# Performance work log

Hardware: AMD Instinct MI355X
Metric: run time of the kernel (lower is better)

Reference implementation:

```python
import jax, jax.numpy as jnp
import numpy as np

OUT_FEATURES = 64
KERNEL_DIMS = 16


def setup_inputs() -> dict:
    key = jax.random.key(0)
    k1, k2, k3, k4 = jax.random.split(key, 4)
    N, L, F = 256, 64, 32            # in_features = L*F = 2048
    OK = OUT_FEATURES * KERNEL_DIMS  # 1024
    x = jax.random.normal(k1, (N, L, F), dtype=jnp.float32)
    W = jax.random.normal(k2, (OK, L * F), dtype=jnp.float32) * 0.02
    b = jax.random.normal(k3, (OK,), dtype=jnp.float32) * 0.02
    u = jax.random.normal(k4, (OK,), dtype=jnp.float32)
    return {"x": x, "W": W, "b": b, "u": u}


def _l2normalize(a, eps=1e-12):
    return a / (jnp.linalg.norm(a) + eps)


def reference(x, W, b, u):
    N, L, F = x.shape
    xf = x.reshape(N, L * F)
    # spectral norm: one power iteration (u, v detached, as in torch)
    W_ng = jax.lax.stop_gradient(W)
    v = _l2normalize(W_ng.T @ u)
    u_new = _l2normalize(W_ng @ v)
    sigma = u_new @ (W @ v)          # differentiable in W
    W_sn = W / sigma
    # projection: (N, out, k)
    m = (xf @ W_sn.T + b).reshape(N, OUT_FEATURES, KERNEL_DIMS)
    # all-pairs L1 distance over kernel dim -> (N, N, out)
    norm = jnp.abs(m[:, None, :, :] - m[None, :, :, :]).sum(-1)
    o_b = jnp.exp(-norm).sum(0) - 1.0          # (N, out); self term exp(0)=1 removed
    o_b = jnp.broadcast_to(o_b[:, None, :], (N, L, OUT_FEATURES))
    return jnp.concatenate([x, o_b], axis=-1)  # (N, L, F + out)
```

## Files before the change

kernel.cpp:

```cpp
#include <hip/hip_runtime.h>
#include <hip/hip_bf16.h>
#include <math.h>

#define KIN  2048
#define OKD  1024
#define NB   256
#define OUTF 64
#define KD   16

typedef float f32x4  __attribute__((ext_vector_type(4)));
typedef short bf16x4 __attribute__((ext_vector_type(4)));
typedef short bf16x8 __attribute__((ext_vector_type(8)));
typedef unsigned short u16x8 __attribute__((ext_vector_type(8)));

static __device__ __forceinline__ unsigned short f2bf(float f) {
    union { __hip_bfloat16 b; unsigned short u; } cv;
    cv.b = __float2bfloat16(f);
    return cv.u;
}
static __device__ __forceinline__ u16x8 pack8(float4 a, float4 b) {
    u16x8 r;
    r[0]=f2bf(a.x); r[1]=f2bf(a.y); r[2]=f2bf(a.z); r[3]=f2bf(a.w);
    r[4]=f2bf(b.x); r[5]=f2bf(b.y); r[6]=f2bf(b.z); r[7]=f2bf(b.w);
    return r;
}
static __device__ __forceinline__ float bf2f(unsigned short u) {
    union { unsigned int i; float f; } cv; cv.i = ((unsigned int)u) << 16; return cv.f;
}

__global__ __launch_bounds__(256) void k_stage1(const float* __restrict__ W,
        const float* __restrict__ u, const float* __restrict__ x,
        float* __restrict__ partial, unsigned short* __restrict__ Wb,
        unsigned short* __restrict__ xb, float4* __restrict__ out4) {
    int bid = blockIdx.x, tid = threadIdx.x;
    if (bid < 256) {
        int row0 = bid * 4;
        int c = tid * 8;
        float s[8];
#pragma unroll
        for (int i = 0; i < 8; ++i) s[i] = 0.f;
#pragma unroll
        for (int r = 0; r < 4; ++r) {
            int row = row0 + r;
            const float4* src = (const float4*)(W + (size_t)row * KIN + c);
            float4 f0 = src[0], f1 = src[1];
            *(u16x8*)(Wb + (size_t)row * KIN + c) = pack8(f0, f1);
            float uu = u[row];
            s[0] += f0.x * uu; s[1] += f0.y * uu; s[2] += f0.z * uu; s[3] += f0.w * uu;
            s[4] += f1.x * uu; s[5] += f1.y * uu; s[6] += f1.z * uu; s[7] += f1.w * uu;
        }
        float4* dst = (float4*)(partial + (size_t)bid * KIN + c);
        dst[0] = make_float4(s[0], s[1], s[2], s[3]);
        dst[1] = make_float4(s[4], s[5], s[6], s[7]);
    } else if (bid < 288) {
        int xc = bid - 256;
        const float4* x4 = (const float4*)x;
#pragma unroll
        for (int p = 0; p < 8; ++p) {
            int g = xc * 2048 + p * 256 + tid;
            float4 f0 = x4[(size_t)g * 2], f1 = x4[(size_t)g * 2 + 1];
            *((u16x8*)xb + g) = pack8(f0, f1);
        }
    } else {
        int xo = bid - 288;
        const float4* x4 = (const float4*)x;
#pragma unroll
        for (int p = 0; p < 4; ++p) {
            int i = xo * 1024 + p * 256 + tid;
            int r = i >> 3, c = i & 7;
            out4[(size_t)r * 24 + c] = x4[i];
        }
    }
}

__global__ __launch_bounds__(256) void k_vred(const float* __restrict__ partial,
                                              float* __restrict__ partial2) {
    int bid = blockIdx.x, tid = threadIdx.x;
    int bg = bid & 1, cg = bid >> 1;
    int col = cg * 256 + tid;
    float a = 0.f;
#pragma unroll 8
    for (int i = 0; i < 128; ++i)
        a += partial[(size_t)(bg * 128 + i) * KIN + col];
    partial2[bg * KIN + col] = a;
}

static __device__ __forceinline__ bf16x8 load_frag(const unsigned short* lds, int row, int k0) {
    int b0 = (row << 7) + (k0 << 1);
    b0 ^= (row & 7) << 4;
    bf16x4 lo = *(const bf16x4*)((const char*)lds + b0);
    bf16x4 hi = *(const bf16x4*)((const char*)lds + (b0 ^ 32));
    bf16x8 r;
    r[0]=lo[0]; r[1]=lo[1]; r[2]=lo[2]; r[3]=lo[3];
    r[4]=hi[0]; r[5]=hi[1]; r[6]=hi[2]; r[7]=hi[3];
    return r;
}

__global__ __launch_bounds__(256) void k_tg(const unsigned short* __restrict__ xb,
        const unsigned short* __restrict__ Wb, const float* __restrict__ partial2,
        float* __restrict__ tpart, float* __restrict__ P) {
    __shared__ unsigned short sAB[2][4096];
    __shared__ float part[4], part2s[4];
    int bid = blockIdx.x, tid = threadIdx.x;
    int lane = tid & 63, w = tid >> 6;

    if (bid >= 256) {
        int tb = bid - 256;
        int row = tb * 2 + (w >> 1);
        int h = w & 1;
        const u16x8* W8 = (const u16x8*)(Wb + (size_t)row * KIN + h * 1024);
        const float4* pa = (const float4*)(partial2 + h * 1024);
        const float4* pb = (const float4*)(partial2 + KIN + h * 1024);
        float s = 0.f, s2 = 0.f;
#pragma unroll
        for (int q = 0; q < 2; ++q) {
            int idx = q * 64 + lane;
            u16x8 a = W8[idx];
            float4 a0 = pa[idx * 2], a1 = pa[idx * 2 + 1];
            float4 b0 = pb[idx * 2], b1 = pb[idx * 2 + 1];
            float v0 = a0.x + b0.x, v1 = a0.y + b0.y, v2 = a0.z + b0.z, v3 = a0.w + b0.w;
            float v4 = a1.x + b1.x, v5 = a1.y + b1.y, v6 = a1.z + b1.z, v7 = a1.w + b1.w;
            s += bf2f(a[0])*v0 + bf2f(a[1])*v1 + bf2f(a[2])*v2 + bf2f(a[3])*v3;
            s += bf2f(a[4])*v4 + bf2f(a[5])*v5 + bf2f(a[6])*v6 + bf2f(a[7])*v7;
            s2 += v0*v0 + v1*v1 + v2*v2 + v3*v3 + v4*v4 + v5*v5 + v6*v6 + v7*v7;
        }
#pragma unroll
        for (int off = 32; off; off >>= 1) { s += __shfl_xor(s, off); s2 += __shfl_xor(s2, off); }
        if (lane == 0) { part[w] = s; part2s[w] = s2; }
        __syncthreads();
        if (tid == 0) {
            float r0 = part[0] + part[1], r1 = part[2] + part[3];
            tpart[tb] = r0 * r0 + r1 * r1;
            if (tb == 0) tpart[512] = part2s[0] + part2s[1];
        }
        return;
    }

    int c0 = (bid & 31) * 32, n0 = (bid >> 5) * 32;

    const char* gq[2];
    int lqo[2];
#pragma unroll
    for (int q = 0; q < 2; ++q) {
        int ch = q * 4 + w;
        int p = ch * 1024 + lane * 16;
        int rp = p & 4095;
        int row = rp >> 7;
        int off = (rp & 127) ^ ((row & 7) << 4);
        const unsigned short* base = (p < 4096) ? xb : Wb;
        int grow = (p < 4096) ? (n0 + row) : (c0 + row);
        gq[q] = (const char*)(base + (size_t)grow * KIN) + off;
        lqo[q] = ch * 512;
    }

    int g = lane >> 4, cl = lane & 15;
    int wy = w >> 1, wx = w & 1;
    f32x4 acc;
#pragma unroll
    for (int r = 0; r < 4; ++r) acc[r] = 0.f;

#pragma unroll
    for (int q = 0; q < 2; ++q)
        __builtin_amdgcn_global_load_lds(
            (const __attribute__((address_space(1))) unsigned int*)(gq[q]),
            (__attribute__((address_space(3))) unsigned int*)(&sAB[0][lqo[q]]), 16, 0, 0);
    __syncthreads();

    for (int t = 0; t < 32; ++t) {
        int cur = t & 1;
        if (t < 31) {
            int kb = (t + 1) * 128;
#pragma unroll
            for (int q = 0; q < 2; ++q)
                __builtin_amdgcn_global_load_lds(
                    (const __attribute__((address_space(1))) unsigned int*)(gq[q] + kb),
                    (__attribute__((address_space(3))) unsigned int*)(&sAB[cur ^ 1][lqo[q]]), 16, 0, 0);
        }
        const unsigned short* sA = sAB[cur];
        const unsigned short* sB = sAB[cur] + 2048;
#pragma unroll
        for (int s = 0; s < 2; ++s) {
            int k0 = s * 32 + 4 * g;
            bf16x8 af = load_frag(sA, wy * 16 + cl, k0);
            bf16x8 bf = load_frag(sB, wx * 16 + cl, k0);
            acc = __builtin_amdgcn_mfma_f32_16x16x32_bf16(af, bf, acc, 0, 0, 0);
        }
        __syncthreads();
    }

    int col = c0 + wx * 16 + cl;
    int row0 = n0 + wy * 16 + 4 * g;
#pragma unroll
    for (int r = 0; r < 4; ++r)
        P[(size_t)(row0 + r) * OKD + col] = acc[r];
}

__global__ __launch_bounds__(256) void k_pair(const float* __restrict__ M,
        const float* __restrict__ tpart, float* __restrict__ ob) {
    __shared__ float sm[NB * KD];
    __shared__ float sred[4];
    int o = blockIdx.x, tid = threadIdx.x;

    float tv = tpart[tid] + tpart[tid + 256];
#pragma unroll
    for (int off = 32; off; off >>= 1) tv += __shfl_xor(tv, off);
    if ((tid & 63) == 0) sred[tid >> 6] = tv;

    const float4* M4 = (const float4*)M;
    float4* sm4 = (float4*)sm;
#pragma unroll
    for (int tq = 0; tq < 4; ++tq) {
        int idx = tid + tq * 256;
        int j = idx >> 2, k4 = idx & 3;
        sm4[j * 4 + (k4 ^ (j & 3))] = M4[(size_t)j * 256 + o * 4 + k4];
    }
    __syncthreads();

    float ssum = sred[0] + sred[1] + sred[2] + sred[3];
    float nv2 = tpart[512];
    float ssq = ssum / nv2;
    float invs = (sqrtf(ssq) + 1e-12f) / ssq;

    int n = blockIdx.y * 32 + (tid >> 3);
    int jc = tid & 7;
    int nx = (n & 3) << 2;
    float r[KD];
#pragma unroll
    for (int k = 0; k < KD; ++k) r[k] = sm[n * 16 + (k ^ nx)];
    float acc = 0.f;
    for (int jj = 0; jj < 32; ++jj) {
        int j = jj * 8 + jc;
        int base = j * 16, jx = (j & 3) << 2;
        float d = 0.f;
#pragma unroll
        for (int k = 0; k < KD; ++k) d += fabsf(r[k] - sm[base + (k ^ jx)]);
        acc += __expf(-d * invs);
    }
    acc += __shfl_xor(acc, 1);
    acc += __shfl_xor(acc, 2);
    acc += __shfl_xor(acc, 4);
    if (jc == 0) ob[n * OUTF + o] = acc - 1.0f;
}

__global__ void k_obout(const float* __restrict__ ob, float4* __restrict__ out4) {
    int bid = blockIdx.x, tid = threadIdx.x;
    const float4* ob4 = (const float4*)ob;
#pragma unroll
    for (int p = 0; p < 4; ++p) {
        int i = bid * 1024 + p * 256 + tid;
        int r = i >> 4, c2 = i & 15;
        out4[(size_t)r * 24 + 8 + c2] = ob4[(r >> 6) * 16 + c2];
    }
}

extern "C" void kernel_launch(void* const* d_in, const int* in_sizes, int n_in,
                              void* d_out, int out_size, void* d_ws, size_t ws_size,
                              hipStream_t stream) {
    const float* x = (const float*)d_in[0];
    const float* W = (const float*)d_in[1];
    const float* u = (const float*)d_in[3];

    float* ws = (float*)d_ws;
    float* partial  = ws;
    float* P        = ws;
    float* partial2 = ws + 524288;
    float* tpart    = ws + 528384;
    float* ob       = ws + 529408;
    unsigned short* Wb = (unsigned short*)(ws + 545792);
    unsigned short* xb = (unsigned short*)(ws + 1594368);

    k_stage1<<<416, 256, 0, stream>>>(W, u, x, partial, Wb, xb, (float4*)d_out);
    k_vred  <<<16,  256, 0, stream>>>(partial, partial2);
    k_tg    <<<768, 256, 0, stream>>>(xb, Wb, partial2, tpart, P);
    k_pair  <<<dim3(64, 8), 256, 0, stream>>>(P, tpart, ob);
    k_obout <<<256, 256, 0, stream>>>(ob, (float4*)d_out);
}
```

Before: 102.3 us.

## Fuse all stages into one cooperative persistent kernel with grid syncs

```diff
diff --git a/kernel.cpp b/kernel.cpp
--- a/kernel.cpp
+++ b/kernel.cpp
@@ -1,6 +1,9 @@
 #include <hip/hip_runtime.h>
+#include <hip/hip_cooperative_groups.h>
 #include <hip/hip_bf16.h>
 #include <math.h>
+
+namespace cg = cooperative_groups;
 
 #define KIN  2048
 #define OKD  1024
@@ -26,63 +29,6 @@
 }
 static __device__ __forceinline__ float bf2f(unsigned short u) {
     union { unsigned int i; float f; } cv; cv.i = ((unsigned int)u) << 16; return cv.f;
-}
-
-__global__ __launch_bounds__(256) void k_stage1(const float* __restrict__ W,
-        const float* __restrict__ u, const float* __restrict__ x,
-        float* __restrict__ partial, unsigned short* __restrict__ Wb,
-        unsigned short* __restrict__ xb, float4* __restrict__ out4) {
-    int bid = blockIdx.x, tid = threadIdx.x;
-    if (bid < 256) {
-        int row0 = bid * 4;
-        int c = tid * 8;
-        float s[8];
-#pragma unroll
-        for (int i = 0; i < 8; ++i) s[i] = 0.f;
-#pragma unroll
-        for (int r = 0; r < 4; ++r) {
-            int row = row0 + r;
-            const float4* src = (const float4*)(W + (size_t)row * KIN + c);
-            float4 f0 = src[0], f1 = src[1];
-            *(u16x8*)(Wb + (size_t)row * KIN + c) = pack8(f0, f1);
-            float uu = u[row];
-            s[0] += f0.x * uu; s[1] += f0.y * uu; s[2] += f0.z * uu; s[3] += f0.w * uu;
-            s[4] += f1.x * uu; s[5] += f1.y * uu; s[6] += f1.z * uu; s[7] += f1.w * uu;
-        }
-        float4* dst = (float4*)(partial + (size_t)bid * KIN + c);
-        dst[0] = make_float4(s[0], s[1], s[2], s[3]);
-        dst[1] = make_float4(s[4], s[5], s[6], s[7]);
-    } else if (bid < 288) {
-        int xc = bid - 256;
-        const float4* x4 = (const float4*)x;
-#pragma unroll
-        for (int p = 0; p < 8; ++p) {
-            int g = xc * 2048 + p * 256 + tid;
-            float4 f0 = x4[(size_t)g * 2], f1 = x4[(size_t)g * 2 + 1];
-            *((u16x8*)xb + g) = pack8(f0, f1);
-        }
-    } else {
-        int xo = bid - 288;
-        const float4* x4 = (const float4*)x;
-#pragma unroll
-        for (int p = 0; p < 4; ++p) {
-            int i = xo * 1024 + p * 256 + tid;
-            int r = i >> 3, c = i & 7;
-            out4[(size_t)r * 24 + c] = x4[i];
-        }
-    }
-}
-
-__global__ __launch_bounds__(256) void k_vred(const float* __restrict__ partial,
-                                              float* __restrict__ partial2) {
-    int bid = blockIdx.x, tid = threadIdx.x;
-    int bg = bid & 1, cg = bid >> 1;
-    int col = cg * 256 + tid;
-    float a = 0.f;
-#pragma unroll 8
-    for (int i = 0; i < 128; ++i)
-        a += partial[(size_t)(bg * 128 + i) * KIN + col];
-    partial2[bg * KIN + col] = a;
 }
 
 static __device__ __forceinline__ bf16x8 load_frag(const unsigned short* lds, int row, int k0) {
@@ -96,160 +42,214 @@
     return r;
 }
 
-__global__ __launch_bounds__(256) void k_tg(const unsigned short* __restrict__ xb,
-        const unsigned short* __restrict__ Wb, const float* __restrict__ partial2,
-        float* __restrict__ tpart, float* __restrict__ P) {
-    __shared__ unsigned short sAB[2][4096];
-    __shared__ float part[4], part2s[4];
+__global__ __launch_bounds__(256) void k_mega(
+        const float* __restrict__ W, const float* __restrict__ u,
+        const float* __restrict__ x,
+        float* __restrict__ partial, float* __restrict__ vraw,
+        float* __restrict__ nvpart, float* __restrict__ tpart,
+        float* __restrict__ P, unsigned short* __restrict__ Wb,
+        unsigned short* __restrict__ xb, float* __restrict__ outF) {
+    cg::grid_group grid = cg::this_grid();
+    __shared__ __align__(16) unsigned char SMEM[16384];
+    __shared__ float small_[16];
+
     int bid = blockIdx.x, tid = threadIdx.x;
     int lane = tid & 63, w = tid >> 6;
-
-    if (bid >= 256) {
-        int tb = bid - 256;
-        int row = tb * 2 + (w >> 1);
-        int h = w & 1;
-        const u16x8* W8 = (const u16x8*)(Wb + (size_t)row * KIN + h * 1024);
-        const float4* pa = (const float4*)(partial2 + h * 1024);
-        const float4* pb = (const float4*)(partial2 + KIN + h * 1024);
-        float s = 0.f, s2 = 0.f;
-#pragma unroll
-        for (int q = 0; q < 2; ++q) {
+    const float4* x4 = (const float4*)x;
+    float4* out4 = (float4*)outF;
+
+    {
+        int c = tid * 8;
+        float s[8];
+#pragma unroll
+        for (int i = 0; i < 8; ++i) s[i] = 0.f;
+#pragma unroll
+        for (int r = 0; r < 4; ++r) {
+            int row = bid * 4 + r;
+            const float4* src = (const float4*)(W + (size_t)row * KIN + c);
+            float4 f0 = src[0], f1 = src[1];
+            *(u16x8*)(Wb + (size_t)row * KIN + c) = pack8(f0, f1);
+            float uu = u[row];
+            s[0] += f0.x * uu; s[1] += f0.y * uu; s[2] += f0.z * uu; s[3] += f0.w * uu;
+            s[4] += f1.x * uu; s[5] += f1.y * uu; s[6] += f1.z * uu; s[7] += f1.w * uu;
+        }
+        float4* dst = (float4*)(partial + (size_t)bid * KIN + c);
+        dst[0] = make_float4(s[0], s[1], s[2], s[3]);
+        dst[1] = make_float4(s[4], s[5], s[6], s[7]);
+
+        int g = bid * 256 + tid;
+        float4 f0 = x4[(size_t)g * 2], f1 = x4[(size_t)g * 2 + 1];
+        *((u16x8*)xb + g) = pack8(f0, f1);
+
+#pragma unroll
+        for (int p = 0; p < 2; ++p) {
+            int i = bid * 512 + p * 256 + tid;
+            int r = i >> 3, cc = i & 7;
+            out4[(size_t)r * 24 + cc] = x4[i];
+        }
+    }
+    grid.sync();
+
+    {
+        int c0 = bid * 8 + w * 2;
+        float a0 = 0.f, a1 = 0.f;
+#pragma unroll
+        for (int q = 0; q < 4; ++q) {
+            const float2 pv = *(const float2*)(partial + (size_t)(lane + 64 * q) * KIN + c0);
+            a0 += pv.x; a1 += pv.y;
+        }
+#pragma unroll
+        for (int off = 32; off; off >>= 1) {
+            a0 += __shfl_xor(a0, off); a1 += __shfl_xor(a1, off);
+        }
+        if (lane == 0) {
+            vraw[c0] = a0; vraw[c0 + 1] = a1;
+            small_[w] = a0 * a0 + a1 * a1;
+        }
+    }
+    __syncthreads();
+    if (tid == 0) nvpart[bid] = small_[0] + small_[1] + small_[2] + small_[3];
+    grid.sync();
+
+    {
+        int row = bid * 4 + w;
+        const u16x8* W8 = (const u16x8*)(Wb + (size_t)row * KIN);
+        const float4* v4 = (const float4*)vraw;
+        float s = 0.f;
+#pragma unroll
+        for (int q = 0; q < 4; ++q) {
             int idx = q * 64 + lane;
             u16x8 a = W8[idx];
-            float4 a0 = pa[idx * 2], a1 = pa[idx * 2 + 1];
-            float4 b0 = pb[idx * 2], b1 = pb[idx * 2 + 1];
-            float v0 = a0.x + b0.x, v1 = a0.y + b0.y, v2 = a0.z + b0.z, v3 = a0.w + b0.w;
-            float v4 = a1.x + b1.x, v5 = a1.y + b1.y, v6 = a1.z + b1.z, v7 = a1.w + b1.w;
-            s += bf2f(a[0])*v0 + bf2f(a[1])*v1 + bf2f(a[2])*v2 + bf2f(a[3])*v3;
-            s += bf2f(a[4])*v4 + bf2f(a[5])*v5 + bf2f(a[6])*v6 + bf2f(a[7])*v7;
-            s2 += v0*v0 + v1*v1 + v2*v2 + v3*v3 + v4*v4 + v5*v5 + v6*v6 + v7*v7;
-        }
-#pragma unroll
-        for (int off = 32; off; off >>= 1) { s += __shfl_xor(s, off); s2 += __shfl_xor(s2, off); }
-        if (lane == 0) { part[w] = s; part2s[w] = s2; }
-        __syncthreads();
-        if (tid == 0) {
-            float r0 = part[0] + part[1], r1 = part[2] + part[3];
-            tpart[tb] = r0 * r0 + r1 * r1;
-            if (tb == 0) tpart[512] = part2s[0] + part2s[1];
-        }
-        return;
-    }
-
-    int c0 = (bid & 31) * 32, n0 = (bid >> 5) * 32;
-
-    const char* gq[2];
-    int lqo[2];
-#pragma unroll
-    for (int q = 0; q < 2; ++q) {
-        int ch = q * 4 + w;
-        int p = ch * 1024 + lane * 16;
-        int rp = p & 4095;
-        int row = rp >> 7;
-        int off = (rp & 127) ^ ((row & 7) << 4);
-        const unsigned short* base = (p < 4096) ? xb : Wb;
-        int grow = (p < 4096) ? (n0 + row) : (c0 + row);
-        gq[q] = (const char*)(base + (size_t)grow * KIN) + off;
-        lqo[q] = ch * 512;
-    }
-
-    int g = lane >> 4, cl = lane & 15;
-    int wy = w >> 1, wx = w & 1;
-    f32x4 acc;
-#pragma unroll
-    for (int r = 0; r < 4; ++r) acc[r] = 0.f;
-
-#pragma unroll
-    for (int q = 0; q < 2; ++q)
-        __builtin_amdgcn_global_load_lds(
-            (const __attribute__((address_space(1))) unsigned int*)(gq[q]),
-            (__attribute__((address_space(3))) unsigned int*)(&sAB[0][lqo[q]]), 16, 0, 0);
+            float4 b0 = v4[idx * 2], b1 = v4[idx * 2 + 1];
+            s += bf2f(a[0])*b0.x + bf2f(a[1])*b0.y + bf2f(a[2])*b0.z + bf2f(a[3])*b0.w;
+            s += bf2f(a[4])*b1.x + bf2f(a[5])*b1.y + bf2f(a[6])*b1.z + bf2f(a[7])*b1.w;
+        }
+#pragma unroll
+        for (int off = 32; off; off >>= 1) s += __shfl_xor(s, off);
+        if (lane == 0) small_[w] = s * s;
+    }
     __syncthreads();
-
-    for (int t = 0; t < 32; ++t) {
-        int cur = t & 1;
-        if (t < 31) {
-            int kb = (t + 1) * 128;
-#pragma unroll
-            for (int q = 0; q < 2; ++q)
-                __builtin_amdgcn_global_load_lds(
-                    (const __attribute__((address_space(1))) unsigned int*)(gq[q] + kb),
-                    (__attribute__((address_space(3))) unsigned int*)(&sAB[cur ^ 1][lqo[q]]), 16, 0, 0);
-        }
-        const unsigned short* sA = sAB[cur];
-        const unsigned short* sB = sAB[cur] + 2048;
-#pragma unroll
-        for (int s = 0; s < 2; ++s) {
-            int k0 = s * 32 + 4 * g;
-            bf16x8 af = load_frag(sA, wy * 16 + cl, k0);
-            bf16x8 bf = load_frag(sB, wx * 16 + cl, k0);
-            acc = __builtin_amdgcn_mfma_f32_16x16x32_bf16(af, bf, acc, 0, 0, 0);
-        }
-        __syncthreads();
-    }
-
-    int col = c0 + wx * 16 + cl;
-    int row0 = n0 + wy * 16 + 4 * g;
-#pragma unroll
-    for (int r = 0; r < 4; ++r)
-        P[(size_t)(row0 + r) * OKD + col] = acc[r];
-}
-
-__global__ __launch_bounds__(256) void k_pair(const float* __restrict__ M,
-        const float* __restrict__ tpart, float* __restrict__ ob) {
-    __shared__ float sm[NB * KD];
-    __shared__ float sred[4];
-    int o = blockIdx.x, tid = threadIdx.x;
-
-    float tv = tpart[tid] + tpart[tid + 256];
-#pragma unroll
-    for (int off = 32; off; off >>= 1) tv += __shfl_xor(tv, off);
-    if ((tid & 63) == 0) sred[tid >> 6] = tv;
-
-    const float4* M4 = (const float4*)M;
-    float4* sm4 = (float4*)sm;
-#pragma unroll
-    for (int tq = 0; tq < 4; ++tq) {
-        int idx = tid + tq * 256;
-        int j = idx >> 2, k4 = idx & 3;
-        sm4[j * 4 + (k4 ^ (j & 3))] = M4[(size_t)j * 256 + o * 4 + k4];
-    }
-    __syncthreads();
-
-    float ssum = sred[0] + sred[1] + sred[2] + sred[3];
-    float nv2 = tpart[512];
-    float ssq = ssum / nv2;
-    float invs = (sqrtf(ssq) + 1e-12f) / ssq;
-
-    int n = blockIdx.y * 32 + (tid >> 3);
-    int jc = tid & 7;
-    int nx = (n & 3) << 2;
-    float r[KD];
-#pragma unroll
-    for (int k = 0; k < KD; ++k) r[k] = sm[n * 16 + (k ^ nx)];
-    float acc = 0.f;
-    for (int jj = 0; jj < 32; ++jj) {
-        int j = jj * 8 + jc;
-        int base = j * 16, jx = (j & 3) << 2;
-        float d = 0.f;
-#pragma unroll
-        for (int k = 0; k < KD; ++k) d += fabsf(r[k] - sm[base + (k ^ jx)]);
-        acc += __expf(-d * invs);
-    }
-    acc += __shfl_xor(acc, 1);
-    acc += __shfl_xor(acc, 2);
-    acc += __shfl_xor(acc, 4);
-    if (jc == 0) ob[n * OUTF + o] = acc - 1.0f;
-}
-
-__global__ void k_obout(const float* __restrict__ ob, float4* __restrict__ out4) {
-    int bid = blockIdx.x, tid = threadIdx.x;
-    const float4* ob4 = (const float4*)ob;
-#pragma unroll
-    for (int p = 0; p < 4; ++p) {
-        int i = bid * 1024 + p * 256 + tid;
-        int r = i >> 4, c2 = i & 15;
-        out4[(size_t)r * 24 + 8 + c2] = ob4[(r >> 6) * 16 + c2];
+    if (tid == 0) tpart[bid] = small_[0] + small_[1] + small_[2] + small_[3];
+    if (bid == 0) {
+        float nv = nvpart[tid];
+#pragma unroll
+        for (int off = 32; off; off >>= 1) nv += __shfl_xor(nv, off);
+        if (lane == 0) small_[8 + w] = nv;
+        __syncthreads();
+        if (tid == 0) tpart[256] = small_[8] + small_[9] + small_[10] + small_[11];
+    }
+    {
+        unsigned short* sAB0 = (unsigned short*)SMEM;
+        int c0 = (bid & 31) * 32, n0 = (bid >> 5) * 32;
+        const char* gq[2];
+        int lqo[2];
+#pragma unroll
+        for (int q = 0; q < 2; ++q) {
+            int ch = q * 4 + w;
+            int p = ch * 1024 + lane * 16;
+            int rp = p & 4095;
+            int row = rp >> 7;
+            int off = (rp & 127) ^ ((row & 7) << 4);
+            const unsigned short* base = (p < 4096) ? xb : Wb;
+            int grow = (p < 4096) ? (n0 + row) : (c0 + row);
+            gq[q] = (const char*)(base + (size_t)grow * KIN) + off;
+            lqo[q] = ch * 512;
+        }
+        int g = lane >> 4, cl = lane & 15;
+        int wy = w >> 1, wx = w & 1;
+        f32x4 acc;
+#pragma unroll
+        for (int r = 0; r < 4; ++r) acc[r] = 0.f;
+
+        __syncthreads();
+#pragma unroll
+        for (int q = 0; q < 2; ++q)
+            __builtin_amdgcn_global_load_lds(
+                (const __attribute__((address_space(1))) unsigned int*)(gq[q]),
+                (__attribute__((address_space(3))) unsigned int*)(sAB0 + lqo[q]), 16, 0, 0);
+        __syncthreads();
+
+        for (int t = 0; t < 32; ++t) {
+            int cur = t & 1;
+            unsigned short* cbuf = sAB0 + (cur << 12);
+            unsigned short* pbuf = sAB0 + ((cur ^ 1) << 12);
+            if (t < 31) {
+                int kb = (t + 1) * 128;
+#pragma unroll
+                for (int q = 0; q < 2; ++q)
+                    __builtin_amdgcn_global_load_lds(
+                        (const __attribute__((address_space(1))) unsigned int*)(gq[q] + kb),
+                        (__attribute__((address_space(3))) unsigned int*)(pbuf + lqo[q]), 16, 0, 0);
+            }
+            const unsigned short* sA = cbuf;
+            const unsigned short* sB = cbuf + 2048;
+#pragma unroll
+            for (int s = 0; s < 2; ++s) {
+                int k0 = s * 32 + 4 * g;
+                bf16x8 af = load_frag(sA, wy * 16 + cl, k0);
+                bf16x8 bf = load_frag(sB, wx * 16 + cl, k0);
+                acc = __builtin_amdgcn_mfma_f32_16x16x32_bf16(af, bf, acc, 0, 0, 0);
+            }
+            __syncthreads();
+        }
+        int col = c0 + wx * 16 + cl;
+        int row0 = n0 + wy * 16 + 4 * g;
+#pragma unroll
+        for (int r = 0; r < 4; ++r)
+            P[(size_t)(row0 + r) * OKD + col] = acc[r];
+    }
+    grid.sync();
+
+    {
+        float* sm = (float*)SMEM;
+        int o = bid & 63, h = bid >> 6;
+
+        float tv = tpart[tid];
+#pragma unroll
+        for (int off = 32; off; off >>= 1) tv += __shfl_xor(tv, off);
+        if (lane == 0) small_[w] = tv;
+
+        const float4* M4 = (const float4*)P;
+        float4* sm4 = (float4*)sm;
+#pragma unroll
+        for (int tq = 0; tq < 4; ++tq) {
+            int idx = tid + tq * 256;
+            int j = idx >> 2, k4 = idx & 3;
+            sm4[j * 4 + (k4 ^ (j & 3))] = M4[(size_t)j * 256 + o * 4 + k4];
+        }
+        __syncthreads();
+
+        float ssum = small_[0] + small_[1] + small_[2] + small_[3];
+        float nv2 = tpart[256];
+        float ssq = ssum / nv2;
+        float invs = (sqrtf(ssq) + 1e-12f) / ssq;
+
+        int nl = tid >> 2, jc = tid & 3;
+        int n = h * 64 + nl;
+        int nx = (n & 3) << 2;
+        float r[KD];
+#pragma unroll
+        for (int k = 0; k < KD; ++k) r[k] = sm[n * 16 + (k ^ nx)];
+        float acc = 0.f;
+        for (int jj = 0; jj < 64; ++jj) {
+            int j = jj * 4 + jc;
+            int base = j * 16, jx = (j & 3) << 2;
+            float d = 0.f;
+#pragma unroll
+            for (int k = 0; k < KD; ++k) d += fabsf(r[k] - sm[base + (k ^ jx)]);
+            acc += __expf(-d * invs);
+        }
+        acc += __shfl_xor(acc, 1);
+        acc += __shfl_xor(acc, 2);
+        __syncthreads();
+        if (jc == 0) sm[nl] = acc - 1.0f;
+        __syncthreads();
+#pragma unroll
+        for (int s5 = 0; s5 < 16; ++s5) {
+            int idx = s5 * 256 + tid;
+            int n2 = idx >> 6, l = idx & 63;
+            outF[(size_t)((h * 64 + n2) * 64 + l) * 96 + 32 + o] = sm[n2];
+        }
     }
 }
 
@@ -261,17 +261,17 @@
     const float* u = (const float*)d_in[3];
 
     float* ws = (float*)d_ws;
-    float* partial  = ws;
-    float* P        = ws;
-    float* partial2 = ws + 524288;
-    float* tpart    = ws + 528384;
-    float* ob       = ws + 529408;
-    unsigned short* Wb = (unsigned short*)(ws + 545792);
-    unsigned short* xb = (unsigned short*)(ws + 1594368);
-
-    k_stage1<<<416, 256, 0, stream>>>(W, u, x, partial, Wb, xb, (float4*)d_out);
-    k_vred  <<<16,  256, 0, stream>>>(partial, partial2);
-    k_tg    <<<768, 256, 0, stream>>>(xb, Wb, partial2, tpart, P);
-    k_pair  <<<dim3(64, 8), 256, 0, stream>>>(P, tpart, ob);
-    k_obout <<<256, 256, 0, stream>>>(ob, (float4*)d_out);
-}
+    float* partial = ws;
+    float* vraw    = ws + 524288;
+    float* nvpart  = ws + 526336;
+    float* tpart   = ws + 526592;
+    float* P       = ws + 528384;
+    unsigned short* Wb = (unsigned short*)(ws + 790528);
+    unsigned short* xb = (unsigned short*)(ws + 1839104);
+    float* outF = (float*)d_out;
+
+    void* args[] = { (void*)&W, (void*)&u, (void*)&x, (void*)&partial,
+                     (void*)&vraw, (void*)&nvpart, (void*)&tpart, (void*)&P,
+                     (void*)&Wb, (void*)&xb, (void*)&outF };
+    hipLaunchCooperativeKernel((void*)k_mega, dim3(256), dim3(256), args, 0, stream);
+}
```

Result: slower. 207.2 us (+102.6%).

## Split GEMM K dimension in two and widen vector reduction partitioning

Applied to the files above, without the earlier changes.

```diff
diff --git a/kernel.cpp b/kernel.cpp
--- a/kernel.cpp
+++ b/kernel.cpp
@@ -74,15 +74,15 @@
 }
 
 __global__ __launch_bounds__(256) void k_vred(const float* __restrict__ partial,
-                                              float* __restrict__ partial2) {
-    int bid = blockIdx.x, tid = threadIdx.x;
-    int bg = bid & 1, cg = bid >> 1;
+                                              float* __restrict__ partial4) {
+    int bid = blockIdx.x, tid = threadIdx.x;
+    int bg = bid >> 3, cg = bid & 7;
     int col = cg * 256 + tid;
     float a = 0.f;
 #pragma unroll 8
-    for (int i = 0; i < 128; ++i)
-        a += partial[(size_t)(bg * 128 + i) * KIN + col];
-    partial2[bg * KIN + col] = a;
+    for (int i = 0; i < 64; ++i)
+        a += partial[(size_t)(bg * 64 + i) * KIN + col];
+    partial4[bg * KIN + col] = a;
 }
 
 static __device__ __forceinline__ bf16x8 load_frag(const unsigned short* lds, int row, int k0) {
@@ -97,32 +97,39 @@
 }
 
 __global__ __launch_bounds__(256) void k_tg(const unsigned short* __restrict__ xb,
-        const unsigned short* __restrict__ Wb, const float* __restrict__ partial2,
+        const unsigned short* __restrict__ Wb, const float* __restrict__ partial4,
         float* __restrict__ tpart, float* __restrict__ P) {
     __shared__ unsigned short sAB[2][4096];
     __shared__ float part[4], part2s[4];
     int bid = blockIdx.x, tid = threadIdx.x;
     int lane = tid & 63, w = tid >> 6;
 
-    if (bid >= 256) {
-        int tb = bid - 256;
+    if (bid >= 512) {
+        int tb = bid - 512;
         int row = tb * 2 + (w >> 1);
         int h = w & 1;
         const u16x8* W8 = (const u16x8*)(Wb + (size_t)row * KIN + h * 1024);
-        const float4* pa = (const float4*)(partial2 + h * 1024);
-        const float4* pb = (const float4*)(partial2 + KIN + h * 1024);
+        const float4* p0 = (const float4*)(partial4 + h * 1024);
+        const float4* p1 = (const float4*)(partial4 + KIN + h * 1024);
+        const float4* p2 = (const float4*)(partial4 + 2 * KIN + h * 1024);
+        const float4* p3 = (const float4*)(partial4 + 3 * KIN + h * 1024);
         float s = 0.f, s2 = 0.f;
 #pragma unroll
         for (int q = 0; q < 2; ++q) {
             int idx = q * 64 + lane;
             u16x8 a = W8[idx];
-            float4 a0 = pa[idx * 2], a1 = pa[idx * 2 + 1];
-            float4 b0 = pb[idx * 2], b1 = pb[idx * 2 + 1];
-            float v0 = a0.x + b0.x, v1 = a0.y + b0.y, v2 = a0.z + b0.z, v3 = a0.w + b0.w;
-            float v4 = a1.x + b1.x, v5 = a1.y + b1.y, v6 = a1.z + b1.z, v7 = a1.w + b1.w;
-            s += bf2f(a[0])*v0 + bf2f(a[1])*v1 + bf2f(a[2])*v2 + bf2f(a[3])*v3;
-            s += bf2f(a[4])*v4 + bf2f(a[5])*v5 + bf2f(a[6])*v6 + bf2f(a[7])*v7;
-            s2 += v0*v0 + v1*v1 + v2*v2 + v3*v3 + v4*v4 + v5*v5 + v6*v6 + v7*v7;
+#pragma unroll
+            for (int e = 0; e < 2; ++e) {
+                float4 a0 = p0[idx * 2 + e], b0 = p1[idx * 2 + e];
+                float4 c0 = p2[idx * 2 + e], d0 = p3[idx * 2 + e];
+                float v0 = a0.x + b0.x + c0.x + d0.x;
+                float v1 = a0.y + b0.y + c0.y + d0.y;
+                float v2 = a0.z + b0.z + c0.z + d0.z;
+                float v3 = a0.w + b0.w + c0.w + d0.w;
+                s += bf2f(a[e*4+0])*v0 + bf2f(a[e*4+1])*v1
+                   + bf2f(a[e*4+2])*v2 + bf2f(a[e*4+3])*v3;
+                s2 += v0*v0 + v1*v1 + v2*v2 + v3*v3;
+            }
         }
 #pragma unroll
         for (int off = 32; off; off >>= 1) { s += __shfl_xor(s, off); s2 += __shfl_xor(s2, off); }
@@ -136,7 +143,8 @@
         return;
     }
 
-    int c0 = (bid & 31) * 32, n0 = (bid >> 5) * 32;
+    int tile = bid & 255, kc = bid >> 8;
+    int c0 = (tile & 31) * 32, n0 = (tile >> 5) * 32;
 
     const char* gq[2];
     int lqo[2];
@@ -149,7 +157,7 @@
         int off = (rp & 127) ^ ((row & 7) << 4);
         const unsigned short* base = (p < 4096) ? xb : Wb;
         int grow = (p < 4096) ? (n0 + row) : (c0 + row);
-        gq[q] = (const char*)(base + (size_t)grow * KIN) + off;
+        gq[q] = (const char*)(base + (size_t)grow * KIN + kc * 1024) + off;
         lqo[q] = ch * 512;
     }
 
@@ -166,9 +174,9 @@
             (__attribute__((address_space(3))) unsigned int*)(&sAB[0][lqo[q]]), 16, 0, 0);
     __syncthreads();
 
-    for (int t = 0; t < 32; ++t) {
+    for (int t = 0; t < 16; ++t) {
         int cur = t & 1;
-        if (t < 31) {
+        if (t < 15) {
             int kb = (t + 1) * 128;
 #pragma unroll
             for (int q = 0; q < 2; ++q)
@@ -190,12 +198,13 @@
 
     int col = c0 + wx * 16 + cl;
     int row0 = n0 + wy * 16 + 4 * g;
+    float* Pk = P + (size_t)kc * (NB * OKD);
 #pragma unroll
     for (int r = 0; r < 4; ++r)
-        P[(size_t)(row0 + r) * OKD + col] = acc[r];
-}
-
-__global__ __launch_bounds__(256) void k_pair(const float* __restrict__ M,
+        Pk[(size_t)(row0 + r) * OKD + col] = acc[r];
+}
+
+__global__ __launch_bounds__(256) void k_pair(const float* __restrict__ P,
         const float* __restrict__ tpart, float* __restrict__ ob) {
     __shared__ float sm[NB * KD];
     __shared__ float sred[4];
@@ -206,13 +215,16 @@
     for (int off = 32; off; off >>= 1) tv += __shfl_xor(tv, off);
     if ((tid & 63) == 0) sred[tid >> 6] = tv;
 
-    const float4* M4 = (const float4*)M;
+    const float4* M4 = (const float4*)P;
     float4* sm4 = (float4*)sm;
 #pragma unroll
     for (int tq = 0; tq < 4; ++tq) {
         int idx = tid + tq * 256;
         int j = idx >> 2, k4 = idx & 3;
-        sm4[j * 4 + (k4 ^ (j & 3))] = M4[(size_t)j * 256 + o * 4 + k4];
+        float4 a = M4[(size_t)j * 256 + o * 4 + k4];
+        float4 b = M4[(size_t)65536 + j * 256 + o * 4 + k4];
+        sm4[j * 4 + (k4 ^ (j & 3))] =
+            make_float4(a.x + b.x, a.y + b.y, a.z + b.z, a.w + b.w);
     }
     __syncthreads();
 
@@ -263,15 +275,15 @@
     float* ws = (float*)d_ws;
     float* partial  = ws;
     float* P        = ws;
-    float* partial2 = ws + 524288;
-    float* tpart    = ws + 528384;
-    float* ob       = ws + 529408;
-    unsigned short* Wb = (unsigned short*)(ws + 545792);
-    unsigned short* xb = (unsigned short*)(ws + 1594368);
-
-    k_stage1<<<416, 256, 0, stream>>>(W, u, x, partial, Wb, xb, (float4*)d_out);
-    k_vred  <<<16,  256, 0, stream>>>(partial, partial2);
-    k_tg    <<<768, 256, 0, stream>>>(xb, Wb, partial2, tpart, P);
+    float* partial4 = ws + 524288;
+    float* tpart    = ws + 532480;
+    float* ob       = ws + 533504;
+    unsigned short* Wb = (unsigned short*)(ws + 549888);
+    unsigned short* xb = (unsigned short*)(ws + 1598464);
+
+    k_stage1<<<416,  256, 0, stream>>>(W, u, x, partial, Wb, xb, (float4*)d_out);
+    k_vred  <<<32,   256, 0, stream>>>(partial, partial4);
+    k_tg    <<<1024, 256, 0, stream>>>(xb, Wb, partial4, tpart, P);
     k_pair  <<<dim3(64, 8), 256, 0, stream>>>(P, tpart, ob);
-    k_obout <<<256, 256, 0, stream>>>(ob, (float4*)d_out);
-}
+    k_obout <<<256,  256, 0, stream>>>(ob, (float4*)d_out);
+}
```

Result: faster. 93.68 us (-8.4%).
